# Kernel tuning notes

Measured on AMD Instinct MI355X. Metric: run time of the kernel, lower is better.

The kernel has to match this reference:

```python
import jax, jax.numpy as jnp
import numpy as np

B, S, N, E = 16, 2048, 256, 4096      # batch, tokens, max entities, edges per sample
H, LD, ETR = 512, 16, 768             # hidden_size, label_emb_dim, transformer dim
D = H + LD                            # graph_dim = 528
C1 = 3                                # num_edge_classes + 1
GL = 2                                # gcn_layers
NLBL = 15                             # num_node_classes + 2


def setup_inputs() -> dict:
    key = jax.random.key(0)
    ks = jax.random.split(key, 14)
    s = 0.02
    inp = {}
    inp["emb"] = jax.random.normal(ks[0], (B, S, ETR), jnp.float32)
    inp["ent_indices"] = jax.random.randint(ks[1], (B, S), 0, N + 1)
    inp["ent_labels"] = jax.random.randint(ks[2], (B, N), 0, NLBL)
    inp["edge_index"] = jax.random.randint(ks[3], (B, 2, E), 0, N + 1)
    inp["edge_attr"] = jax.random.randint(ks[4], (B, E), 0, C1)
    inp["cands"] = jax.random.randint(ks[5], (B, N + 1, N + 1), 0, 2).astype(bool)
    inp["W_red"] = jax.random.normal(ks[6], (ETR, H), jnp.float32) * s
    inp["b_red"] = jnp.zeros((H,), jnp.float32)
    inp["emb_label_tbl"] = jax.random.normal(ks[7], (NLBL, LD), jnp.float32) * s
    inp["W_gcn"] = jax.random.normal(ks[8], (C1, GL, D, D), jnp.float32) * s
    inp["b_gcn"] = jnp.zeros((C1, GL, D), jnp.float32)
    inp["W_head"] = jax.random.normal(ks[9], (D, D), jnp.float32) * s
    inp["b_head"] = jnp.zeros((D,), jnp.float32)
    inp["W_tail"] = jax.random.normal(ks[10], (D, D), jnp.float32) * s
    inp["b_tail"] = jnp.zeros((D,), jnp.float32)
    inp["W_out"] = jax.random.normal(ks[11], (D, C1), jnp.float32) * s
    inp["b_out"] = jnp.zeros((C1,), jnp.float32)
    return inp


def _gcn_layer(x, src, dst, w_e, W, b):
    """PyG GCNConv with edge weights w_e (0/1 relation mask) and self loops.
    x: [n, D]; src/dst: [E]; aggregation flow source->target."""
    n = x.shape[0]
    h = x @ W
    deg = jax.ops.segment_sum(w_e, dst, num_segments=n) + 1.0  # +1 self loop
    dinv = jax.lax.rsqrt(deg)
    coef = w_e * dinv[src] * dinv[dst]                         # D^-1/2 A D^-1/2
    agg = jax.ops.segment_sum(coef[:, None] * h[src], dst, num_segments=n)
    return agg + h / deg[:, None] + b                          # self-loop norm = 1/deg


def reference(emb, ent_indices, ent_labels, edge_index, edge_attr, cands,
              W_red, b_red, emb_label_tbl, W_gcn, b_gcn,
              W_head, b_head, W_tail, b_tail, W_out, b_out):
    n_nodes = cands.shape[1]  # max_num_ent + 1
    # fc_reduction of frozen transformer embeddings
    red = emb @ W_red + b_red                                   # [B,S,H]
    # tag-based segment aggregation: max over (mask * emb) == max(segment_max, 0)
    seg_max = jax.vmap(lambda e, ids: jax.ops.segment_max(e, ids, num_segments=n_nodes))(red, ent_indices)
    ent_hidden = jnp.maximum(seg_max, 0.0).at[:, 0, :].set(0.0)  # tag 0 stays zero
    # label embeddings: tag t uses ent_labels[:, t-1]; zeroed where label==0
    lab = emb_label_tbl[ent_labels] * (ent_labels != 0)[..., None].astype(red.dtype)
    lab0 = jnp.broadcast_to(emb_label_tbl[0], (lab.shape[0], 1, lab.shape[-1]))
    label_part = jnp.concatenate([lab0, lab], axis=1)           # [B,n_nodes,LD]
    x0 = jnp.concatenate([label_part, ent_hidden], axis=-1)     # [B,n_nodes,D]
    # multi-relation GCN: per edge class, stacked GCNConv, summed then averaged
    src, dst = edge_index[:, 0], edge_index[:, 1]
    layer_v = jax.vmap(_gcn_layer, in_axes=(0, 0, 0, 0, None, None))
    result = jnp.zeros_like(x0)
    n_cls = W_gcn.shape[0]
    for c in range(n_cls):
        w_e = (edge_attr == c).astype(x0.dtype)
        x = x0
        for l in range(W_gcn.shape[1]):
            x = layer_v(x, src, dst, w_e, W_gcn[c, l], b_gcn[c, l])
        result = result + x
    result = result / n_cls
    # head/tail projections and 'add' pairwise features gated by candidate mask
    x_head = result @ W_head + b_head
    x_tail = result @ W_tail + b_tail
    m = cands[:, :, 1:].astype(x0.dtype)                        # [B,n_nodes,n_nodes-1]
    # fc_out is linear: ((h_i + t_j) * m_ij) @ W + b == m_ij*(hW_i + tW_j) + b
    hW = x_head @ W_out                                         # [B,n_nodes,C1]
    tW = x_tail[:, 1:] @ W_out                                  # [B,n_nodes-1,C1]
    logits = (hW[:, :, None, :] + tW[:, None, :, :]) * m[..., None] + b_out
    return logits  # [B, n_nodes, n_nodes-1, C1] edge-class logits
```

## Files before the change

kernel.cpp:

```cpp
#include <hip/hip_runtime.h>
#include <hip/hip_bf16.h>

typedef unsigned short u16;
typedef __attribute__((ext_vector_type(8))) short short8;
typedef __attribute__((ext_vector_type(4))) float floatx4;

#define B_ 16
#define S_ 2048
#define NNODE 257
#define E_ 4096
#define ETR_ 768
#define H_ 512
#define D_ 528
#define KPAD 544
#define NC 3
#define NROW (B_*NNODE)
#define DD (D_*D_)

#define BM 128
#define BN 128
#define BK 32

__device__ inline u16 f2b(float x) {
    __hip_bfloat16 h = __float2bfloat16(x);
    return *(u16*)&h;
}
__device__ inline float b2f(u16 u) {
    return __uint_as_float(((unsigned)u) << 16);
}

__device__ inline void gll16(const u16* g, u16* l) {
    __builtin_amdgcn_global_load_lds(
        (const __attribute__((address_space(1))) void*)g,
        (__attribute__((address_space(3))) void*)l,
        16, 0, 0);
}

__device__ inline int clampi(int v, int hi) { return v < hi ? v : hi; }

__global__ void transpose_cvt(const float* __restrict__ in, u16* __restrict__ out,
                              int R, int Cc, size_t instride, size_t outstride,
                              int opitch)
{
    __shared__ float t[32][33];
    const int z = blockIdx.z;
    const int tx = threadIdx.x & 31, ty = threadIdx.x >> 5;
    const int c0 = blockIdx.x * 32, r0 = blockIdx.y * 32;
    const float* ip = in + z * instride;
    u16* op = out + z * outstride;
#pragma unroll
    for (int i = 0; i < 4; i++) {
        const int r = r0 + ty + i * 8, c = c0 + tx;
        if (r < R && c < Cc) t[ty + i * 8][tx] = ip[(size_t)r * Cc + c];
    }
    __syncthreads();
#pragma unroll
    for (int i = 0; i < 4; i++) {
        const int c = c0 + ty + i * 8, r = r0 + tx;
        if (c < Cc && r < R) op[(size_t)c * opitch + r] = f2b(t[tx][ty + i * 8]);
    }
}

template<int SWZ, int OB16>
__global__ __launch_bounds__(256)
void gemm_mfma(const float* __restrict__ A, const u16* __restrict__ Wt,
               const float* __restrict__ bias_base, size_t bias_stride,
               void* __restrict__ Cv, int M, int N, int K, float scale,
               size_t astride, size_t wstride, size_t cstride, int cpitch)
{
    __shared__ u16 SS[8192];
    const int tid = threadIdx.x;
    const int wave = tid >> 6, lane = tid & 63;
    const int quad = lane >> 4, l16 = lane & 15;
    const int z = blockIdx.z;
    int bx = blockIdx.x, by = blockIdx.y;
    if (SWZ) {
        const int lin = blockIdx.x + (blockIdx.y << 2);
        bx = (lin >> 3) & 3;
        by = (lin & 7) + ((lin >> 5) << 3);
    }
    const int m0 = by * BM, n0 = bx * BN;

    floatx4 acc[2][8];
#pragma unroll
    for (int t = 0; t < 2; t++)
#pragma unroll
        for (int u = 0; u < 8; u++)
#pragma unroll
            for (int r = 0; r < 4; r++) acc[t][u][r] = 0.f;

    const int srow = tid >> 2;
    const int scol = (tid & 3) * 8;
    const float* aF0 = A + z * astride + (size_t)clampi(m0 + srow,      M - 1) * K + scol;
    const float* aF1 = A + z * astride + (size_t)clampi(m0 + 64 + srow, M - 1) * K + scol;
    const u16* bP0 = Wt + z * wstride + (size_t)clampi(n0 + srow,      N - 1) * K + scol;
    const u16* bP1 = Wt + z * wstride + (size_t)clampi(n0 + 64 + srow, N - 1) * K + scol;
    u16* const ls = &SS[0] + wave * 512;
    u16* const aw0 = &SS[srow * 32 + scol];
    u16* const aw1 = &SS[2048 + srow * 32 + scol];

    for (int k0 = 0; k0 < K; k0 += BK) {
        const float4 v0 = *(const float4*)(aF0 + k0);
        const float4 v1 = *(const float4*)(aF0 + k0 + 4);
        const float4 v2 = *(const float4*)(aF1 + k0);
        const float4 v3 = *(const float4*)(aF1 + k0 + 4);
        gll16(bP0 + k0, ls + 4096);
        gll16(bP1 + k0, ls + 6144);
        short8 p0, p1;
        p0[0] = (short)f2b(v0.x); p0[1] = (short)f2b(v0.y);
        p0[2] = (short)f2b(v0.z); p0[3] = (short)f2b(v0.w);
        p0[4] = (short)f2b(v1.x); p0[5] = (short)f2b(v1.y);
        p0[6] = (short)f2b(v1.z); p0[7] = (short)f2b(v1.w);
        p1[0] = (short)f2b(v2.x); p1[1] = (short)f2b(v2.y);
        p1[2] = (short)f2b(v2.z); p1[3] = (short)f2b(v2.w);
        p1[4] = (short)f2b(v3.x); p1[5] = (short)f2b(v3.y);
        p1[6] = (short)f2b(v3.z); p1[7] = (short)f2b(v3.w);
        *(short8*)aw0 = p0;
        *(short8*)aw1 = p1;
        __syncthreads();
        short8 af[2], bfv[8];
        af[0] = *(const short8*)&SS[(wave * 32 + l16) * 32 + quad * 8];
        af[1] = *(const short8*)&SS[(wave * 32 + 16 + l16) * 32 + quad * 8];
#pragma unroll
        for (int u = 0; u < 8; u++)
            bfv[u] = *(const short8*)&SS[4096 + (u * 16 + l16) * 32 + quad * 8];
#pragma unroll
        for (int t = 0; t < 2; t++)
#pragma unroll
            for (int u = 0; u < 8; u++)
                acc[t][u] = __builtin_amdgcn_mfma_f32_16x16x32_bf16(af[t], bfv[u], acc[t][u], 0, 0, 0);
        __syncthreads();
    }

    const float* bias = bias_base ? (bias_base + z * bias_stride) : nullptr;
#pragma unroll
    for (int t = 0; t < 2; t++) {
#pragma unroll
        for (int r = 0; r < 4; r++) {
            const int m = m0 + wave * 32 + t * 16 + quad * 4 + r;
            if (m >= M) continue;
#pragma unroll
            for (int u = 0; u < 8; u++) {
                const int n = n0 + u * 16 + l16;
                if (n < N) {
                    const float v = acc[t][u][r] * scale + (bias ? bias[n] : 0.f);
                    if (OB16) {
                        u16* Cb = (u16*)Cv;
                        Cb[z * cstride + (size_t)m * cpitch + n] = f2b(v);
                    } else {
                        float* Cf = (float*)Cv;
                        Cf[z * cstride + (size_t)m * cpitch + n] = v;
                    }
                }
            }
        }
    }
}

template<int MODE>
__global__ __launch_bounds__(256)
void gemm64(const float* __restrict__ A, const float* __restrict__ W,
            const float* __restrict__ bias, float* __restrict__ C,
            int M, int N, int K, float scale,
            const int* __restrict__ segidx, float* __restrict__ segout)
{
    __shared__ float Asl[16][68];
    __shared__ float Bsl[16][64];
    const int tid = threadIdx.x;
    const int tx = tid & 15, ty = tid >> 4;
    const int m0 = blockIdx.y * 64, n0 = blockIdx.x * 64;
    const int arow = tid >> 2, acol = (tid & 3) * 4;
    const int brow = tid >> 4, bcol = (tid & 15) * 4;

    float acc[4][4];
#pragma unroll
    for (int i = 0; i < 4; i++)
#pragma unroll
        for (int j = 0; j < 4; j++) acc[i][j] = 0.f;

    for (int kk = 0; kk < K; kk += 16) {
        float4 av = make_float4(0.f, 0.f, 0.f, 0.f);
        if (m0 + arow < M) av = *(const float4*)(A + (size_t)(m0 + arow) * K + kk + acol);
        Asl[acol + 0][arow] = av.x; Asl[acol + 1][arow] = av.y;
        Asl[acol + 2][arow] = av.z; Asl[acol + 3][arow] = av.w;
        float4 bv = make_float4(0.f, 0.f, 0.f, 0.f);
        if (n0 + bcol < N) bv = *(const float4*)(W + (size_t)(kk + brow) * N + n0 + bcol);
        *(float4*)&Bsl[brow][bcol] = bv;
        __syncthreads();
#pragma unroll
        for (int k = 0; k < 16; k++) {
            const float4 a = *(const float4*)&Asl[k][ty * 4];
            const float4 b = *(const float4*)&Bsl[k][tx * 4];
            const float af[4] = { a.x, a.y, a.z, a.w };
            const float bfv[4] = { b.x, b.y, b.z, b.w };
#pragma unroll
            for (int i = 0; i < 4; i++)
#pragma unroll
                for (int j = 0; j < 4; j++) acc[i][j] += af[i] * bfv[j];
        }
        __syncthreads();
    }

#pragma unroll
    for (int i = 0; i < 4; i++) {
        const int m = m0 + ty * 4 + i;
        if (m >= M) continue;
        if (MODE == 1) {
            const int bb = m >> 11;
            const int idx = segidx[m];
            float* const srow = segout + (((size_t)bb * NNODE + idx) << 9);
#pragma unroll
            for (int j = 0; j < 4; j++) {
                const int n = n0 + tx * 4 + j;
                const float v = acc[i][j] + (bias ? bias[n] : 0.f);
                atomicMax(((int*)srow) + n, __float_as_int(v));
            }
        } else {
#pragma unroll
            for (int j = 0; j < 4; j++) {
                const int n = n0 + tx * 4 + j;
                if (n < N) {
                    const float v = acc[i][j] * scale + (bias ? bias[n] : 0.f);
                    C[(size_t)m * N + n] = v;
                }
            }
        }
    }
}

__global__ void rows_csr(const int* __restrict__ ent_indices,
                         int* __restrict__ rptr, int* __restrict__ rlist)
{
    __shared__ int cnt[NNODE];
    const int b = blockIdx.x;
    const int tid = threadIdx.x;
    const int* idx = ent_indices + (size_t)b * S_;
    for (int i = tid; i < NNODE; i += 256) cnt[i] = 0;
    __syncthreads();
    for (int r = tid; r < S_; r += 256) atomicAdd(&cnt[idx[r]], 1);
    __syncthreads();
    if (tid == 0) {
        int run = 0;
        for (int i = 0; i < NNODE; i++) { const int c = cnt[i]; cnt[i] = run; run += c; }
    }
    __syncthreads();
    for (int i = tid; i < NNODE; i += 256) rptr[b * (NNODE + 1) + i] = cnt[i];
    if (tid == 0) rptr[b * (NNODE + 1) + NNODE] = S_;
    __syncthreads();
    for (int r = tid; r < S_; r += 256) {
        const int pos = atomicAdd(&cnt[idx[r]], 1);
        rlist[(size_t)b * S_ + pos] = r;
    }
}

__global__ __launch_bounds__(256)
void segmax_x0(const u16* __restrict__ redC, const int* __restrict__ rptr,
               const int* __restrict__ rlist, const float* __restrict__ b_red,
               const int* __restrict__ ent_labels, const float* __restrict__ tbl,
               u16* __restrict__ x0b)
{
    const int bn = blockIdx.x;
    const int b = bn / NNODE, n = bn % NNODE;
    const int tid = threadIdx.x;
    const int c0 = tid * 2;
    const int start = rptr[b * (NNODE + 1) + n];
    const int end   = (n == 0) ? start : rptr[b * (NNODE + 1) + n + 1];
    float m0 = -INFINITY, m1 = -INFINITY;
    const int* rl = rlist + (size_t)b * S_;
    for (int i = start; i < end; i++) {
        const u16* row = redC + ((size_t)b * S_ + rl[i]) * H_;
        const unsigned v = *(const unsigned*)(row + c0);
        m0 = fmaxf(m0, __uint_as_float((v & 0xffffu) << 16));
        m1 = fmaxf(m1, __uint_as_float(v & 0xffff0000u));
    }
    float h0, h1;
    if (n == 0) { h0 = 0.f; h1 = 0.f; }
    else {
        h0 = fmaxf(m0 + b_red[c0], 0.f);
        h1 = fmaxf(m1 + b_red[c0 + 1], 0.f);
    }
    u16* orow = x0b + (size_t)bn * KPAD;
    *(unsigned*)(orow + 16 + c0) = (unsigned)f2b(h0) | ((unsigned)f2b(h1) << 16);
    if (tid < 16) {
        float v;
        if (n == 0) v = tbl[tid];
        else {
            const int lab = ent_labels[b * (NNODE - 1) + (n - 1)];
            v = (lab != 0) ? tbl[lab * 16 + tid] : 0.f;
        }
        orow[tid] = f2b(v);
    } else if (tid < 32) {
        orow[512 + tid] = 0;
    }
}

template<int OUTB>
__global__ void build_x0(const float* __restrict__ seg, const int* __restrict__ ent_labels,
                         const float* __restrict__ tbl, float* __restrict__ x0f,
                         u16* __restrict__ x0b)
{
    const int bn = blockIdx.x;
    const int b = bn / NNODE, n = bn % NNODE;
    const int CMAX = OUTB ? KPAD : D_;
    for (int col = threadIdx.x; col < CMAX; col += blockDim.x) {
        float v;
        if (col >= D_) {
            v = 0.f;
        } else if (col < 16) {
            if (n == 0) v = tbl[col];
            else {
                const int lab = ent_labels[b * (NNODE - 1) + (n - 1)];
                v = (lab != 0) ? tbl[lab * 16 + col] : 0.f;
            }
        } else {
            v = (n == 0) ? 0.f : seg[(((size_t)b * NNODE + n) << 9) + (col - 16)];
        }
        if (OUTB) x0b[(size_t)bn * KPAD + col] = f2b(v);
        else      x0f[(size_t)bn * D_ + col] = v;
    }
}

__global__ void csr_build(const int* __restrict__ edge_index, const int* __restrict__ edge_attr,
                          float* __restrict__ degf, int* __restrict__ csr_ptr,
                          int2* __restrict__ csr_sc)
{
    __shared__ int cnt[NC * NNODE];
    __shared__ float dinvl[NC * NNODE];
    const int b = blockIdx.x;
    const int tid = threadIdx.x;
    const int* src = edge_index + (size_t)b * 2 * E_;
    const int* dst = src + E_;
    const int* attr = edge_attr + (size_t)b * E_;

    for (int i = tid; i < NC * NNODE; i += 256) cnt[i] = 0;
    __syncthreads();
    for (int e = tid; e < E_; e += 256) atomicAdd(&cnt[attr[e] * NNODE + dst[e]], 1);
    __syncthreads();
    for (int i = tid; i < NC * NNODE; i += 256) {
        const float d = (float)cnt[i] + 1.0f;
        degf[(size_t)b * NC * NNODE + i] = d;
        dinvl[i] = rsqrtf(d);
    }
    __syncthreads();
    if (tid == 0) {
        int run = 0;
        for (int i = 0; i < NC * NNODE; i++) { const int c = cnt[i]; cnt[i] = run; run += c; }
    }
    __syncthreads();
    for (int i = tid; i < NC * NNODE; i += 256) csr_ptr[(size_t)b * NC * NNODE + i] = cnt[i];
    __syncthreads();
    for (int e = tid; e < E_; e += 256) {
        const int a = attr[e], d = dst[e], s = src[e];
        const int pos = atomicAdd(&cnt[a * NNODE + d], 1);
        const float cf = dinvl[a * NNODE + s] * dinvl[a * NNODE + d];
        csr_sc[(size_t)b * E_ + pos] = make_int2(s, __float_as_int(cf));
    }
}

__global__ __launch_bounds__(256)
void gcn_agg(const u16* __restrict__ x, size_t xzstride,
             const float* __restrict__ degf,
             const int* __restrict__ csr_ptr, const int2* __restrict__ csr_sc,
             float* __restrict__ y)
{
    const int bn = blockIdx.x;
    const int cls = blockIdx.y;
    const int b = bn / NNODE, n = bn % NNODE;
    const int tid = threadIdx.x;
    const int base = b * NC * NNODE + cls * NNODE + n;
    const float d = degf[base];
    const int start = csr_ptr[base];
    const int cnt = (int)d - 1;
    const float inv = 1.0f / d;
    const u16* xp = x + cls * xzstride;
    const u16* xrow = xp + (size_t)bn * KPAD;
    const int c0 = tid, c1 = tid + 256, c2 = tid + 512;
    float a0 = b2f(xrow[c0]) * inv;
    float a1 = b2f(xrow[c1]) * inv;
    float a2 = (c2 < D_) ? b2f(xrow[c2]) * inv : 0.f;
    const int2* scp = csr_sc + (size_t)b * E_ + start;
    int2 sc = (cnt > 0) ? scp[0] : make_int2(0, 0);
    for (int i = 0; i < cnt; i++) {
        const int2 cur = sc;
        if (i + 1 < cnt) sc = scp[i + 1];
        const float cf = __int_as_float(cur.y);
        const u16* xs = xp + ((size_t)b * NNODE + cur.x) * KPAD;
        a0 += cf * b2f(xs[c0]);
        a1 += cf * b2f(xs[c1]);
        if (c2 < D_) a2 += cf * b2f(xs[c2]);
    }
    float* yr = y + ((size_t)cls * NROW + bn) * KPAD;
    yr[c0] = a0; yr[c1] = a1;
    if (c2 < KPAD) yr[c2] = a2;
}

template<int OUT>
__global__ __launch_bounds__(256)
void gcn_gather(const float* __restrict__ h, size_t hstride,
                const float* __restrict__ degf,
                const int* __restrict__ csr_ptr, const int2* __restrict__ csr_sc,
                const float* __restrict__ bias_base, size_t bias_stride,
                float* __restrict__ outf, u16* __restrict__ outb, size_t ostride,
                int cls0)
{
    const int bn = blockIdx.x;
    const int cls = cls0 + blockIdx.y;
    const int b = bn / NNODE, n = bn % NNODE;
    const int tid = threadIdx.x;
    const int base = b * NC * NNODE + cls * NNODE + n;
    const float d = degf[base];
    const int start = csr_ptr[base];
    const int cnt = (int)d - 1;
    const float inv = 1.0f / d;
    const float* hp = h + blockIdx.y * hstride;
    const float* bias = bias_base + cls * bias_stride;
    const float* hrow = hp + (size_t)bn * D_;
    const int c0 = tid, c1 = tid + 256, c2 = tid + 512;
    float a0 = hrow[c0] * inv + bias[c0];
    float a1 = hrow[c1] * inv + bias[c1];
    float a2 = (c2 < D_) ? hrow[c2] * inv + bias[c2] : 0.f;
    const int2* scp = csr_sc + (size_t)b * E_ + start;
    for (int i = 0; i < cnt; i++) {
        const int2 sc = scp[i];
        const float cf = __int_as_float(sc.y);
        const float* hs = hp + ((size_t)b * NNODE + sc.x) * D_;
        a0 += cf * hs[c0];
        a1 += cf * hs[c1];
        if (c2 < D_) a2 += cf * hs[c2];
    }
    if (OUT == 1) {
        float* orow = outf + (size_t)bn * D_;
        orow[c0] += a0; orow[c1] += a1; if (c2 < D_) orow[c2] += a2;
    } else {
        float* orow = outf + (size_t)bn * D_;
        orow[c0] = a0; orow[c1] = a1; if (c2 < D_) orow[c2] = a2;
    }
}

__global__ void rowdot3(const float* __restrict__ x, const float* __restrict__ w,
                        float* __restrict__ out)
{
    const int row = blockIdx.x;
    const int lane = threadIdx.x;
    float a0 = 0.f, a1 = 0.f, a2 = 0.f;
    for (int d = lane; d < D_; d += 64) {
        const float xv = x[(size_t)row * D_ + d];
        a0 += xv * w[d * 3 + 0];
        a1 += xv * w[d * 3 + 1];
        a2 += xv * w[d * 3 + 2];
    }
#pragma unroll
    for (int off = 32; off > 0; off >>= 1) {
        a0 += __shfl_down(a0, off, 64);
        a1 += __shfl_down(a1, off, 64);
        a2 += __shfl_down(a2, off, 64);
    }
    if (lane == 0) {
        out[(size_t)row * 3 + 0] = a0;
        out[(size_t)row * 3 + 1] = a1;
        out[(size_t)row * 3 + 2] = a2;
    }
}

__global__ void prep_heads(const float* __restrict__ W_head, const float* __restrict__ W_tail,
                           const float* __restrict__ b_head, const float* __restrict__ b_tail,
                           const float* __restrict__ W_out,
                           float* __restrict__ Whw, float* __restrict__ Wtw,
                           float* __restrict__ bias6)
{
    const int r = blockIdx.x;
    const int lane = threadIdx.x;
    const float* x; float* o;
    if (r < D_)            { x = W_head + (size_t)r * D_;        o = Whw + (size_t)r * 3; }
    else if (r < 2 * D_)   { x = W_tail + (size_t)(r - D_) * D_; o = Wtw + (size_t)(r - D_) * 3; }
    else if (r == 2 * D_)  { x = b_head;                         o = bias6; }
    else                   { x = b_tail;                         o = bias6 + 3; }
    float a0 = 0.f, a1 = 0.f, a2 = 0.f;
    for (int d = lane; d < D_; d += 64) {
        const float xv = x[d];
        a0 += xv * W_out[d * 3 + 0];
        a1 += xv * W_out[d * 3 + 1];
        a2 += xv * W_out[d * 3 + 2];
    }
#pragma unroll
    for (int off = 32; off > 0; off >>= 1) {
        a0 += __shfl_down(a0, off, 64);
        a1 += __shfl_down(a1, off, 64);
        a2 += __shfl_down(a2, off, 64);
    }
    if (lane == 0) { o[0] = a0; o[1] = a1; o[2] = a2; }
}

__global__ __launch_bounds__(256)
void rowdot6(const float* __restrict__ x3, size_t zstride,
             const float* __restrict__ Whw, const float* __restrict__ Wtw,
             const float* __restrict__ bias6,
             float* __restrict__ hw, float* __restrict__ tw)
{
    const int row = blockIdx.x * 4 + (threadIdx.x >> 6);
    const int lane = threadIdx.x & 63;
    const float* p0 = x3 + (size_t)row * D_;
    const float* p1 = p0 + zstride;
    const float* p2 = p1 + zstride;
    float h0 = 0.f, h1 = 0.f, h2 = 0.f, t0 = 0.f, t1 = 0.f, t2 = 0.f;
    for (int d = lane; d < D_; d += 64) {
        const float xv = (p0[d] + p1[d] + p2[d]) * (1.f / 3.f);
        h0 += xv * Whw[d * 3 + 0]; h1 += xv * Whw[d * 3 + 1]; h2 += xv * Whw[d * 3 + 2];
        t0 += xv * Wtw[d * 3 + 0]; t1 += xv * Wtw[d * 3 + 1]; t2 += xv * Wtw[d * 3 + 2];
    }
#pragma unroll
    for (int off = 32; off > 0; off >>= 1) {
        h0 += __shfl_down(h0, off, 64); h1 += __shfl_down(h1, off, 64); h2 += __shfl_down(h2, off, 64);
        t0 += __shfl_down(t0, off, 64); t1 += __shfl_down(t1, off, 64); t2 += __shfl_down(t2, off, 64);
    }
    if (lane == 0) {
        hw[(size_t)row * 3 + 0] = h0 + bias6[0];
        hw[(size_t)row * 3 + 1] = h1 + bias6[1];
        hw[(size_t)row * 3 + 2] = h2 + bias6[2];
        tw[(size_t)row * 3 + 0] = t0 + bias6[3];
        tw[(size_t)row * 3 + 1] = t1 + bias6[4];
        tw[(size_t)row * 3 + 2] = t2 + bias6[5];
    }
}

__global__ __launch_bounds__(256)
void final_logits(const float* __restrict__ hw, const float* __restrict__ tw,
                  const int* __restrict__ cands, const float* __restrict__ b_out,
                  float* __restrict__ out)
{
    const int bi = blockIdx.x;
    const int b = bi / NNODE;
    const int j = threadIdx.x;
    const float h0 = hw[bi * 3 + 0], h1 = hw[bi * 3 + 1], h2 = hw[bi * 3 + 2];
    const int tj = b * NNODE + 1 + j;
    const float t0 = tw[tj * 3 + 0], t1 = tw[tj * 3 + 1], t2 = tw[tj * 3 + 2];
    const float m = (cands[(size_t)bi * NNODE + 1 + j] != 0) ? 1.f : 0.f;
    const float bo0 = b_out[0], bo1 = b_out[1], bo2 = b_out[2];
    const size_t o = ((size_t)bi * 256 + j) * 3;
    out[o + 0] = (h0 + t0) * m + bo0;
    out[o + 1] = (h1 + t1) * m + bo1;
    out[o + 2] = (h2 + t2) * m + bo2;
}

extern "C" void kernel_launch(void* const* d_in, const int* in_sizes, int n_in,
                              void* d_out, int out_size, void* d_ws, size_t ws_size,
                              hipStream_t stream)
{
    const float* emb       = (const float*)d_in[0];
    const int* ent_indices = (const int*)d_in[1];
    const int* ent_labels  = (const int*)d_in[2];
    const int* edge_index  = (const int*)d_in[3];
    const int* edge_attr   = (const int*)d_in[4];
    const int* cands       = (const int*)d_in[5];
    const float* W_red     = (const float*)d_in[6];
    const float* b_red     = (const float*)d_in[7];
    const float* tbl       = (const float*)d_in[8];
    const float* W_gcn     = (const float*)d_in[9];
    const float* b_gcn     = (const float*)d_in[10];
    const float* W_head    = (const float*)d_in[11];
    const float* b_head    = (const float*)d_in[12];
    const float* W_tail    = (const float*)d_in[13];
    const float* b_tail    = (const float*)d_in[14];
    const float* W_out     = (const float*)d_in[15];
    const float* b_out     = (const float*)d_in[16];

    char* ws = (char*)d_ws;
    size_t off = 0;
    auto alloc = [&](size_t nbytes) -> char* {
        char* p = ws + off; off = (off + nbytes + 255) & ~(size_t)255; return p;
    };
    const size_t ROWB  = (size_t)NROW * D_ * sizeof(float);
    const size_t RD    = (size_t)NROW * D_;
    const size_t RD2   = (size_t)NROW * KPAD;
    const size_t WGZ   = (size_t)2 * D_ * KPAD;

    float* ybuf   = (float*)alloc((size_t)NC * RD2 * 4);
    u16*  x1b     = (u16*)alloc((size_t)NC * RD2 * 2);
    char* R1      = alloc((size_t)B_ * S_ * H_ * sizeof(u16));
    u16*  redC    = (u16*)R1;
    float* result3 = (float*)R1;
    int*  rptr    = (int*)alloc((size_t)B_ * (NNODE + 1) * 4);
    int*  rlist   = (int*)alloc((size_t)B_ * S_ * 4);
    u16*  x0b     = (u16*)alloc((size_t)NROW * KPAD * sizeof(u16));
    u16*  wredT   = (u16*)alloc((size_t)H_ * ETR_ * sizeof(u16));
    u16*  wgcnT   = (u16*)alloc((size_t)NC * WGZ * sizeof(u16));
    float* Whw    = (float*)alloc((size_t)D_ * 3 * 4);
    float* Wtw    = (float*)alloc((size_t)D_ * 3 * 4);
    float* bias6  = (float*)alloc(6 * 4);
    float* degf   = (float*)alloc((size_t)B_ * NC * NNODE * 4);
    float* hwp    = (float*)alloc((size_t)NROW * 3 * 4);
    float* twp    = (float*)alloc((size_t)NROW * 3 * 4);
    int* csr_ptr  = (int*)alloc((size_t)B_ * NC * NNODE * 4);
    int2* csr_sc  = (int2*)alloc((size_t)B_ * E_ * 8);
    const bool fast = (ws_size >= off);

    if (fast) {
        transpose_cvt<<<dim3(16, 24, 1), 256, 0, stream>>>(W_red, wredT, ETR_, H_, 0, 0, ETR_);
        hipMemsetAsync(wgcnT, 0, (size_t)NC * WGZ * sizeof(u16), stream);
        transpose_cvt<<<dim3(17, 17, 6), 256, 0, stream>>>(W_gcn, wgcnT, D_, D_, DD, (size_t)D_ * KPAD, KPAD);

        prep_heads<<<2 * D_ + 2, 64, 0, stream>>>(W_head, W_tail, b_head, b_tail, W_out,
                                                  Whw, Wtw, bias6);

        rows_csr<<<B_, 256, 0, stream>>>(ent_indices, rptr, rlist);
        csr_build<<<B_, 256, 0, stream>>>(edge_index, edge_attr, degf, csr_ptr, csr_sc);

        gemm_mfma<1, 1><<<dim3(H_ / BN, (B_ * S_) / BM, 1), 256, 0, stream>>>(
            emb, wredT, nullptr, 0, redC, B_ * S_, H_, ETR_, 1.f, 0, 0, 0, H_);
        segmax_x0<<<B_ * NNODE, 256, 0, stream>>>(redC, rptr, rlist, b_red,
                                                  ent_labels, tbl, x0b);

        gcn_agg<<<dim3(NROW, NC), 256, 0, stream>>>(x0b, 0, degf, csr_ptr, csr_sc, ybuf);
        dim3 gmm((D_ + BN - 1) / BN, (NROW + BM - 1) / BM, NC);
        gemm_mfma<0, 1><<<gmm, 256, 0, stream>>>(
            ybuf, wgcnT, b_gcn, (size_t)2 * D_, x1b, NROW, D_, KPAD, 1.f,
            RD2, WGZ, RD2, KPAD);
        gcn_agg<<<dim3(NROW, NC), 256, 0, stream>>>(x1b, RD2, degf, csr_ptr, csr_sc, ybuf);
        gemm_mfma<0, 0><<<gmm, 256, 0, stream>>>(
            ybuf, wgcnT + (size_t)D_ * KPAD, b_gcn + D_, (size_t)2 * D_,
            result3, NROW, D_, KPAD, 1.f, RD2, WGZ, RD, D_);

        rowdot6<<<NROW / 4, 256, 0, stream>>>(result3, RD, Whw, Wtw, bias6, hwp, twp);
        final_logits<<<NROW, 256, 0, stream>>>(hwp, twp, cands, b_out, (float*)d_out);
        return;
    }

    off = 0;
    float* bufA = (float*)alloc(ROWB);
    float* bufB = (float*)alloc(ROWB);
    float* bufC = (float*)alloc(ROWB);
    float* bufD = (float*)alloc(ROWB);
    degf = (float*)alloc((size_t)B_ * NC * NNODE * 4);
    hwp  = (float*)alloc((size_t)NROW * 3 * 4);
    twp  = (float*)alloc((size_t)NROW * 3 * 4);
    csr_ptr = (int*)alloc((size_t)B_ * NC * NNODE * 4);
    csr_sc  = (int2*)alloc((size_t)B_ * E_ * 8);

    hipMemsetAsync(bufA, 0, (size_t)B_ * NNODE * H_ * 4, stream);
    hipMemsetAsync(bufD, 0, ROWB, stream);
    gemm64<1><<<dim3(H_ / 64, (B_ * S_) / 64), 256, 0, stream>>>(
        emb, W_red, b_red, nullptr, B_ * S_, H_, ETR_, 1.f, ent_indices, bufA);
    build_x0<0><<<NROW, 256, 0, stream>>>(bufA, ent_labels, tbl, bufB, nullptr);
    csr_build<<<B_, 256, 0, stream>>>(edge_index, edge_attr, degf, csr_ptr, csr_sc);
    dim3 gridG((D_ + 63) / 64, (NROW + 63) / 64);
    for (int c = 0; c < NC; c++) {
        gemm64<0><<<gridG, 256, 0, stream>>>(bufB, W_gcn + (size_t)(c * 2 + 0) * DD,
            nullptr, bufA, NROW, D_, D_, 1.f, nullptr, nullptr);
        gcn_gather<2><<<dim3(NROW, 1), 256, 0, stream>>>(bufA, 0, degf, csr_ptr, csr_sc,
            b_gcn, (size_t)2 * D_, bufC, nullptr, 0, c);
        gemm64<0><<<gridG, 256, 0, stream>>>(bufC, W_gcn + (size_t)(c * 2 + 1) * DD,
            nullptr, bufA, NROW, D_, D_, 1.f, nullptr, nullptr);
        gcn_gather<1><<<dim3(NROW, 1), 256, 0, stream>>>(bufA, 0, degf, csr_ptr, csr_sc,
            b_gcn + D_, (size_t)2 * D_, bufD, nullptr, 0, c);
    }
    gemm64<0><<<gridG, 256, 0, stream>>>(bufD, W_head, b_head, bufB,
        NROW, D_, D_, 1.f / 3.f, nullptr, nullptr);
    gemm64<0><<<gridG, 256, 0, stream>>>(bufD, W_tail, b_tail, bufC,
        NROW, D_, D_, 1.f / 3.f, nullptr, nullptr);
    rowdot3<<<NROW, 64, 0, stream>>>(bufB, W_out, hwp);
    rowdot3<<<NROW, 64, 0, stream>>>(bufC, W_out, twp);
    final_logits<<<NROW, 256, 0, stream>>>(hwp, twp, cands, b_out, (float*)d_out);
}
```

Measured before the change: 450.9 us.

## Pre-convert GEMM A operands to bf16 and load them via global_load_lds

Adds a standalone pass that converts the fp32 embedding to bf16, and makes gcn_agg write bf16 output instead of fp32. All GEMMs now take bf16 A and stage both operands straight into LDS with global_load_lds, dropping the per-tile register conversion. This cuts GEMM read traffic and VALU work, but adds a full read-write pass over the large embedding tensor. Workspace buffers are reorganised so the bf16 embedding aliases the aggregation buffers.

```diff
diff --git a/kernel.cpp b/kernel.cpp
--- a/kernel.cpp
+++ b/kernel.cpp
@@ -38,6 +38,17 @@
 
 __device__ inline int clampi(int v, int hi) { return v < hi ? v : hi; }
 
+__global__ void cvt_bf16(const float* __restrict__ in, u16* __restrict__ out, int n4)
+{
+    const int i = blockIdx.x * 256 + threadIdx.x;
+    if (i < n4) {
+        const float4 f = ((const float4*)in)[i];
+        ushort4 o;
+        o.x = f2b(f.x); o.y = f2b(f.y); o.z = f2b(f.z); o.w = f2b(f.w);
+        ((ushort4*)out)[i] = o;
+    }
+}
+
 __global__ void transpose_cvt(const float* __restrict__ in, u16* __restrict__ out,
                               int R, int Cc, size_t instride, size_t outstride,
                               int opitch)
@@ -63,7 +74,7 @@
 
 template<int SWZ, int OB16>
 __global__ __launch_bounds__(256)
-void gemm_mfma(const float* __restrict__ A, const u16* __restrict__ Wt,
+void gemm_mfma(const u16* __restrict__ A, const u16* __restrict__ Wt,
                const float* __restrict__ bias_base, size_t bias_stride,
                void* __restrict__ Cv, int M, int N, int K, float scale,
                size_t astride, size_t wstride, size_t cstride, int cpitch)
@@ -91,32 +102,17 @@
 
     const int srow = tid >> 2;
     const int scol = (tid & 3) * 8;
-    const float* aF0 = A + z * astride + (size_t)clampi(m0 + srow,      M - 1) * K + scol;
-    const float* aF1 = A + z * astride + (size_t)clampi(m0 + 64 + srow, M - 1) * K + scol;
+    const u16* aP0 = A + z * astride + (size_t)clampi(m0 + srow,      M - 1) * K + scol;
+    const u16* aP1 = A + z * astride + (size_t)clampi(m0 + 64 + srow, M - 1) * K + scol;
     const u16* bP0 = Wt + z * wstride + (size_t)clampi(n0 + srow,      N - 1) * K + scol;
     const u16* bP1 = Wt + z * wstride + (size_t)clampi(n0 + 64 + srow, N - 1) * K + scol;
     u16* const ls = &SS[0] + wave * 512;
-    u16* const aw0 = &SS[srow * 32 + scol];
-    u16* const aw1 = &SS[2048 + srow * 32 + scol];
 
     for (int k0 = 0; k0 < K; k0 += BK) {
-        const float4 v0 = *(const float4*)(aF0 + k0);
-        const float4 v1 = *(const float4*)(aF0 + k0 + 4);
-        const float4 v2 = *(const float4*)(aF1 + k0);
-        const float4 v3 = *(const float4*)(aF1 + k0 + 4);
+        gll16(aP0 + k0, ls);
+        gll16(aP1 + k0, ls + 2048);
         gll16(bP0 + k0, ls + 4096);
         gll16(bP1 + k0, ls + 6144);
-        short8 p0, p1;
-        p0[0] = (short)f2b(v0.x); p0[1] = (short)f2b(v0.y);
-        p0[2] = (short)f2b(v0.z); p0[3] = (short)f2b(v0.w);
-        p0[4] = (short)f2b(v1.x); p0[5] = (short)f2b(v1.y);
-        p0[6] = (short)f2b(v1.z); p0[7] = (short)f2b(v1.w);
-        p1[0] = (short)f2b(v2.x); p1[1] = (short)f2b(v2.y);
-        p1[2] = (short)f2b(v2.z); p1[3] = (short)f2b(v2.w);
-        p1[4] = (short)f2b(v3.x); p1[5] = (short)f2b(v3.y);
-        p1[6] = (short)f2b(v3.z); p1[7] = (short)f2b(v3.w);
-        *(short8*)aw0 = p0;
-        *(short8*)aw1 = p1;
         __syncthreads();
         short8 af[2], bfv[8];
         af[0] = *(const short8*)&SS[(wave * 32 + l16) * 32 + quad * 8];
@@ -361,7 +357,7 @@
 void gcn_agg(const u16* __restrict__ x, size_t xzstride,
              const float* __restrict__ degf,
              const int* __restrict__ csr_ptr, const int2* __restrict__ csr_sc,
-             float* __restrict__ y)
+             u16* __restrict__ y)
 {
     const int bn = blockIdx.x;
     const int cls = blockIdx.y;
@@ -389,9 +385,9 @@
         a1 += cf * b2f(xs[c1]);
         if (c2 < D_) a2 += cf * b2f(xs[c2]);
     }
-    float* yr = y + ((size_t)cls * NROW + bn) * KPAD;
-    yr[c0] = a0; yr[c1] = a1;
-    if (c2 < KPAD) yr[c2] = a2;
+    u16* yr = y + ((size_t)cls * NROW + bn) * KPAD;
+    yr[c0] = f2b(a0); yr[c1] = f2b(a1);
+    if (c2 < KPAD) yr[c2] = (c2 < D_) ? f2b(a2) : 0;
 }
 
 template<int OUT>
@@ -574,8 +570,10 @@
     const size_t RD2   = (size_t)NROW * KPAD;
     const size_t WGZ   = (size_t)2 * D_ * KPAD;
 
-    float* ybuf   = (float*)alloc((size_t)NC * RD2 * 4);
-    u16*  x1b     = (u16*)alloc((size_t)NC * RD2 * 2);
+    char* R0      = alloc((size_t)B_ * S_ * ETR_ * sizeof(u16));
+    u16*  emb_bf  = (u16*)R0;
+    u16*  ybuf_b  = (u16*)R0;
+    u16*  x1b     = (u16*)(R0 + (size_t)16 * 1024 * 1024);
     char* R1      = alloc((size_t)B_ * S_ * H_ * sizeof(u16));
     u16*  redC    = (u16*)R1;
     float* result3 = (float*)R1;
@@ -595,6 +593,8 @@
     const bool fast = (ws_size >= off);
 
     if (fast) {
+        const int n4e = (B_ * S_ * ETR_) / 4;
+        cvt_bf16<<<(n4e + 255) / 256, 256, 0, stream>>>(emb, emb_bf, n4e);
         transpose_cvt<<<dim3(16, 24, 1), 256, 0, stream>>>(W_red, wredT, ETR_, H_, 0, 0, ETR_);
         hipMemsetAsync(wgcnT, 0, (size_t)NC * WGZ * sizeof(u16), stream);
         transpose_cvt<<<dim3(17, 17, 6), 256, 0, stream>>>(W_gcn, wgcnT, D_, D_, DD, (size_t)D_ * KPAD, KPAD);
@@ -606,18 +606,18 @@
         csr_build<<<B_, 256, 0, stream>>>(edge_index, edge_attr, degf, csr_ptr, csr_sc);
 
         gemm_mfma<1, 1><<<dim3(H_ / BN, (B_ * S_) / BM, 1), 256, 0, stream>>>(
-            emb, wredT, nullptr, 0, redC, B_ * S_, H_, ETR_, 1.f, 0, 0, 0, H_);
+            emb_bf, wredT, nullptr, 0, redC, B_ * S_, H_, ETR_, 1.f, 0, 0, 0, H_);
         segmax_x0<<<B_ * NNODE, 256, 0, stream>>>(redC, rptr, rlist, b_red,
                                                   ent_labels, tbl, x0b);
 
-        gcn_agg<<<dim3(NROW, NC), 256, 0, stream>>>(x0b, 0, degf, csr_ptr, csr_sc, ybuf);
+        gcn_agg<<<dim3(NROW, NC), 256, 0, stream>>>(x0b, 0, degf, csr_ptr, csr_sc, ybuf_b);
         dim3 gmm((D_ + BN - 1) / BN, (NROW + BM - 1) / BM, NC);
         gemm_mfma<0, 1><<<gmm, 256, 0, stream>>>(
-            ybuf, wgcnT, b_gcn, (size_t)2 * D_, x1b, NROW, D_, KPAD, 1.f,
+            ybuf_b, wgcnT, b_gcn, (size_t)2 * D_, x1b, NROW, D_, KPAD, 1.f,
             RD2, WGZ, RD2, KPAD);
-        gcn_agg<<<dim3(NROW, NC), 256, 0, stream>>>(x1b, RD2, degf, csr_ptr, csr_sc, ybuf);
+        gcn_agg<<<dim3(NROW, NC), 256, 0, stream>>>(x1b, RD2, degf, csr_ptr, csr_sc, ybuf_b);
         gemm_mfma<0, 0><<<gmm, 256, 0, stream>>>(
-            ybuf, wgcnT + (size_t)D_ * KPAD, b_gcn + D_, (size_t)2 * D_,
+            ybuf_b, wgcnT + (size_t)D_ * KPAD, b_gcn + D_, (size_t)2 * D_,
             result3, NROW, D_, KPAD, 1.f, RD2, WGZ, RD, D_);
 
         rowdot6<<<NROW / 4, 256, 0, stream>>>(result3, RD, Whw, Wtw, bias6, hwp, twp);
```

Result: faster. 435.9 us (-3.3%).
